# Kernel optimization log

Hardware: AMD Instinct MI355X
Metric: run time of the kernel (lower is better)

## Reference

```python
import jax, jax.numpy as jnp
import numpy as np

N = 100000
E = 1600000
B = 64
NUM_CLASSES = 10


def setup_inputs() -> dict:
    key = jax.random.key(0)
    ks = jax.random.split(key, 8)
    x = jax.random.normal(ks[0], (N, 5), dtype=jnp.float32)
    edge_index = jax.random.randint(ks[1], (2, E), 0, N, dtype=jnp.int64)
    batch = jnp.sort(jax.random.randint(ks[2], (N,), 0, B, dtype=jnp.int64))

    def glorot(k, fan_in, fan_out):
        s = jnp.sqrt(6.0 / (fan_in + fan_out)).astype(jnp.float32)
        return jax.random.uniform(k, (fan_in, fan_out), jnp.float32, -s, s)

    dims = [(5, 32), (32, 64), (64, 128), (128, 256)]
    Ws = [glorot(jax.random.fold_in(ks[3], i), a, b) for i, (a, b) in enumerate(dims)]
    bs = [jnp.zeros((b,), jnp.float32) for (_, b) in dims]
    fc1_w = glorot(ks[4], 256, 100)
    fc1_b = jnp.zeros((100,), jnp.float32)
    fc2_w = glorot(ks[5], 100, NUM_CLASSES)
    fc2_b = jnp.zeros((NUM_CLASSES,), jnp.float32)
    return {
        'x': x, 'edge_index': edge_index, 'batch': batch,
        'W1': Ws[0], 'b1': bs[0], 'W2': Ws[1], 'b2': bs[1],
        'W3': Ws[2], 'b3': bs[2], 'W4': Ws[3], 'b4': bs[3],
        'fc1_w': fc1_w, 'fc1_b': fc1_b, 'fc2_w': fc2_w, 'fc2_b': fc2_b,
    }


def _gcn_conv(x, W, b, src, dst, dinv):
    h = x @ W                                   # [N, out]
    norm = (dinv[src] * dinv[dst])[:, None]      # [E, 1]
    msg = h[src] * norm                          # gather + scale
    agg = jax.ops.segment_sum(msg, dst, num_segments=N)
    agg = agg + h * (dinv * dinv)[:, None]       # self-loop contribution
    return agg + b


def reference(x, edge_index, batch, W1, b1, W2, b2, W3, b3, W4, b4,
              fc1_w, fc1_b, fc2_w, fc2_b):
    src, dst = edge_index[0], edge_index[1]
    # degree including self-loop
    deg = jax.ops.segment_sum(jnp.ones((E,), jnp.float32), dst, num_segments=N) + 1.0
    dinv = jax.lax.rsqrt(deg)

    h = jax.nn.relu(_gcn_conv(x, W1, b1, src, dst, dinv))
    # mesh_unpool with pool target 0 -> identity
    h = jax.nn.relu(_gcn_conv(h, W2, b2, src, dst, dinv))
    h = jax.nn.relu(_gcn_conv(h, W3, b3, src, dst, dinv))
    h = jax.nn.relu(_gcn_conv(h, W4, b4, src, dst, dinv))

    # global mean pool over graphs
    sums = jax.ops.segment_sum(h, batch, num_segments=B)
    cnt = jax.ops.segment_sum(jnp.ones((N,), jnp.float32), batch, num_segments=B)
    pooled = sums / jnp.maximum(cnt, 1.0)[:, None]

    h = jax.nn.relu(pooled @ fc1_w + fc1_b)
    return jax.nn.log_softmax(h @ fc2_w + fc2_b, axis=-1)
```

## Files before the change

kernel.cpp:

```cpp
#include <hip/hip_runtime.h>
#include <hip/hip_bf16.h>
#include <cmath>

#define NN 100000
#define NE 1600000
#define NBATCH 64
#define NB 391
#define NBP 512
#define BCAP 6144
#define NPAD (NB * BCAP)

typedef __attribute__((ext_vector_type(8))) _Float16 f16x8;
typedef __attribute__((ext_vector_type(4))) float f32x4;
typedef __attribute__((ext_vector_type(2))) float f32x2;

__device__ __forceinline__ void atomAdd(float* p, float v) {
  unsafeAtomicAdd(p, v);
}

__device__ __forceinline__ unsigned char f2fp8(float f) {
  int pk = __builtin_amdgcn_cvt_pk_fp8_f32(f, f, 0, false);
  return (unsigned char)(pk & 0xff);
}

__device__ __forceinline__ void acc16(uint4 v, f32x2* acc) {
  acc[0] += __builtin_amdgcn_cvt_pk_f32_fp8(v.x, false);
  acc[1] += __builtin_amdgcn_cvt_pk_f32_fp8(v.x, true);
  acc[2] += __builtin_amdgcn_cvt_pk_f32_fp8(v.y, false);
  acc[3] += __builtin_amdgcn_cvt_pk_f32_fp8(v.y, true);
  acc[4] += __builtin_amdgcn_cvt_pk_f32_fp8(v.z, false);
  acc[5] += __builtin_amdgcn_cvt_pk_f32_fp8(v.z, true);
  acc[6] += __builtin_amdgcn_cvt_pk_f32_fp8(v.w, false);
  acc[7] += __builtin_amdgcn_cvt_pk_f32_fp8(v.w, true);
}

__global__ __launch_bounds__(256) void k_bin(const int* __restrict__ src,
    const int* __restrict__ dst, int* __restrict__ bucketCnt, unsigned* __restrict__ pairs,
    const float* __restrict__ W2, const float* __restrict__ W3, const float* __restrict__ W4,
    _Float16* __restrict__ Wt2, _Float16* __restrict__ Wt3, _Float16* __restrict__ Wt4) {
  __shared__ int hist[NBP];
  __shared__ int scn[NBP];
  __shared__ int ofs[NBP];
  __shared__ int gbase[NBP];
  __shared__ unsigned buf[4096];
  __shared__ unsigned short bufb[4096];
  const int base = blockIdx.x * 4096;
  const int n = (NE - base < 4096) ? NE - base : 4096;
  for (int i = threadIdx.x; i < NBP; i += 256) hist[i] = 0;
  __syncthreads();

  int myS[16], myD[16];
  int nloc = 0;
  for (int i = threadIdx.x, j = 0; i < n; i += 256, ++j) {
    myS[j] = src[base + i];
    myD[j] = dst[base + i];
    atomicAdd(&hist[myD[j] >> 8], 1);
    nloc = j + 1;
  }
  __syncthreads();

  scn[threadIdx.x] = hist[threadIdx.x];
  scn[threadIdx.x + 256] = hist[threadIdx.x + 256];
  __syncthreads();
  for (int off = 1; off < NBP; off <<= 1) {
    const int i0 = threadIdx.x, i1 = threadIdx.x + 256;
    int t0 = (i0 >= off) ? scn[i0 - off] : 0;
    int t1 = (i1 >= off) ? scn[i1 - off] : 0;
    __syncthreads();
    scn[i0] += t0;
    scn[i1] += t1;
    __syncthreads();
  }
  ofs[threadIdx.x] = scn[threadIdx.x] - hist[threadIdx.x];
  ofs[threadIdx.x + 256] = scn[threadIdx.x + 256] - hist[threadIdx.x + 256];
  for (int b = threadIdx.x; b < NB; b += 256) {
    int c = hist[b];
    if (c) gbase[b] = b * BCAP + atomicAdd(&bucketCnt[b], c);
  }
  __syncthreads();

  for (int j = 0; j < nloc; ++j) {
    int b = myD[j] >> 8;
    int slot = atomicAdd(&ofs[b], 1);
    buf[slot] = ((unsigned)myS[j] << 8) | ((unsigned)myD[j] & 255u);
    bufb[slot] = (unsigned short)b;
  }
  __syncthreads();

  for (int i = threadIdx.x; i < n; i += 256) {
    int b = (int)bufb[i];
    int ex = scn[b] - hist[b];
    pairs[gbase[b] + (i - ex)] = buf[i];
  }

  int idx = blockIdx.x * 256 + threadIdx.x;
  if (idx < 2048) {
    int k = idx / 64, m = idx - k * 64;
    Wt2[m * 32 + k] = (_Float16)W2[idx];
  } else if (idx < 10240) {
    int j = idx - 2048;
    int k = j / 128, m = j - k * 128;
    Wt3[m * 64 + k] = (_Float16)W3[j];
  } else if (idx < 43008) {
    int j = idx - 10240;
    int k = j / 256, m = j - k * 256;
    Wt4[m * 128 + k] = (_Float16)W4[j];
  }
}

__global__ __launch_bounds__(256) void k_cntfill(const unsigned* __restrict__ pairs,
    const int* __restrict__ bucketCnt, const int* __restrict__ batch,
    const float* __restrict__ x, int* __restrict__ rowbeg, int* __restrict__ rowend,
    float* __restrict__ dinv, int* __restrict__ csrc, float* __restrict__ pcnt,
    _Float16* __restrict__ xs8, unsigned char* __restrict__ F0,
    unsigned char* __restrict__ F1, unsigned char* __restrict__ F2) {
  __shared__ int c[256];
  __shared__ int scn[256];
  __shared__ int rowb[256];
  __shared__ int ofs[256];
  __shared__ int h[64];
  const int tid = threadIdx.x;
  c[tid] = 0; ofs[tid] = 0;
  if (tid < 64) h[tid] = 0;
  __syncthreads();
  const int b = blockIdx.x;
  const int s = b * BCAP;
  const int e = s + bucketCnt[b];
  for (int i = s + tid; i < e; i += 256) atomicAdd(&c[pairs[i] & 255u], 1);
  __syncthreads();
  const int v = c[tid];
  const int pv = (v + 3) & ~3;
  scn[tid] = pv;
  __syncthreads();
  for (int off = 1; off < 256; off <<= 1) {
    int t = (tid >= off) ? scn[tid - off] : 0;
    __syncthreads();
    scn[tid] += t;
    __syncthreads();
  }
  rowb[tid] = s + scn[tid] - pv;
  const int node = b * 256 + tid;
  rowbeg[node] = rowb[tid];
  rowend[node] = rowb[tid] + v;
  for (int p = v; p < pv; ++p) csrc[rowb[tid] + p] = NN;
  if (node < NN) {
    const float di = rsqrtf((float)v + 1.0f);
    dinv[node] = di;
    f16x8 o = {0, 0, 0, 0, 0, 0, 0, 0};
    o[0] = (_Float16)(x[(size_t)node * 5 + 0] * di);
    o[1] = (_Float16)(x[(size_t)node * 5 + 1] * di);
    o[2] = (_Float16)(x[(size_t)node * 5 + 2] * di);
    o[3] = (_Float16)(x[(size_t)node * 5 + 3] * di);
    o[4] = (_Float16)(x[(size_t)node * 5 + 4] * di);
    *(f16x8*)(xs8 + (size_t)node * 8) = o;
    atomicAdd(&h[batch[node]], 1);
  }
  if (b == 0 && tid < 15) {
    const uint4 z = make_uint4(0u, 0u, 0u, 0u);
    if (tid < 1)      ((uint4*)(xs8 + (size_t)NN * 8))[tid] = z;
    else if (tid < 3) ((uint4*)(F0 + (size_t)NN * 32))[tid - 1] = z;
    else if (tid < 7) ((uint4*)(F1 + (size_t)NN * 64))[tid - 3] = z;
    else              ((uint4*)(F2 + (size_t)NN * 128))[tid - 7] = z;
  }
  __syncthreads();
  for (int i = s + tid; i < e; i += 256) {
    unsigned p = pairs[i];
    int t = (int)(p & 255u);
    int pos = rowb[t] + atomicAdd(&ofs[t], 1);
    csrc[pos] = (int)(p >> 8);
  }
  if (tid < 64 && h[tid]) atomAdd(&pcnt[tid], (float)h[tid]);
}

struct MegaArgs {
  const _Float16* xs8;
  const int* rowbeg; const int* rowend; const int* csrc;
  const float* dinv;
  const float* W1; const float* b1;
  unsigned char* F0;
  const _Float16* Wt2; const float* b2;
  unsigned char* F1;
  const _Float16* Wt3; const float* b3;
  unsigned char* F2;
  const _Float16* Wt4; const float* b4;
  const int* batch; float* pooled; const float* pcnt;
  const float* fc1w; const float* fc1b; const float* fc2w; const float* fc2b;
  float* out;
};

__global__ __launch_bounds__(256) void kw_l1(MegaArgs a) {
  __shared__ float w_s[160];
  __shared__ float b_s[32];
  const int tid = threadIdx.x;
  if (tid < 160) w_s[tid] = a.W1[tid];
  if (tid < 32) b_s[tid] = a.b1[tid];
  __syncthreads();
  const int r = blockIdx.x * 256 + tid;
  if (r >= NN) return;
  const float di = a.dinv[r];
  const _Float16* xs = a.xs8;
  f16x8 av = *(const f16x8*)(xs + (size_t)r * 8);
  f16x8 a0 = {0,0,0,0,0,0,0,0}, a1 = {0,0,0,0,0,0,0,0};
  f16x8 a2 = {0,0,0,0,0,0,0,0}, a3 = {0,0,0,0,0,0,0,0};
  const int eb = a.rowbeg[r];
  const int nIt = (a.rowend[r] - eb + 3) >> 2;
  const uint4* cp = (const uint4*)(a.csrc + eb);
  uint4 i0 = cp[0], i1 = cp[1];
  int it = 0;
  for (; it + 2 <= nIt; it += 2) {
    const f16x8 f0 = *(const f16x8*)(xs + (size_t)i0.x * 8);
    const f16x8 f1 = *(const f16x8*)(xs + (size_t)i0.y * 8);
    const f16x8 f2 = *(const f16x8*)(xs + (size_t)i0.z * 8);
    const f16x8 f3 = *(const f16x8*)(xs + (size_t)i0.w * 8);
    const f16x8 f4 = *(const f16x8*)(xs + (size_t)i1.x * 8);
    const f16x8 f5 = *(const f16x8*)(xs + (size_t)i1.y * 8);
    const f16x8 f6 = *(const f16x8*)(xs + (size_t)i1.z * 8);
    const f16x8 f7 = *(const f16x8*)(xs + (size_t)i1.w * 8);
    const uint4 n0 = cp[it + 2], n1 = cp[it + 3];
    a0 += f0; a1 += f1; a2 += f2; a3 += f3;
    a0 += f4; a1 += f5; a2 += f6; a3 += f7;
    i0 = n0; i1 = n1;
  }
  if (it < nIt) {
    const f16x8 f0 = *(const f16x8*)(xs + (size_t)i0.x * 8);
    const f16x8 f1 = *(const f16x8*)(xs + (size_t)i0.y * 8);
    const f16x8 f2 = *(const f16x8*)(xs + (size_t)i0.z * 8);
    const f16x8 f3 = *(const f16x8*)(xs + (size_t)i0.w * 8);
    a0 += f0; a1 += f1; a2 += f2; a3 += f3;
  }
  a0 += a1; a2 += a3; a0 += a2; av += a0;
  const float f0 = (float)av[0] * di, f1 = (float)av[1] * di, f2 = (float)av[2] * di,
              f3 = (float)av[3] * di, f4 = (float)av[4] * di;
  float v[32];
#pragma unroll
  for (int j = 0; j < 32; ++j) {
    float s = b_s[j] + f0 * w_s[j] + f1 * w_s[32 + j] + f2 * w_s[64 + j]
                     + f3 * w_s[96 + j] + f4 * w_s[128 + j];
    v[j] = fmaxf(s, 0.f) * di;
  }
  unsigned u[8];
#pragma unroll
  for (int g2 = 0; g2 < 8; ++g2) {
    int uu = 0;
    uu = __builtin_amdgcn_cvt_pk_fp8_f32(v[4 * g2],     v[4 * g2 + 1], uu, false);
    uu = __builtin_amdgcn_cvt_pk_fp8_f32(v[4 * g2 + 2], v[4 * g2 + 3], uu, true);
    u[g2] = (unsigned)uu;
  }
  uint4* op = (uint4*)(a.F0 + (size_t)r * 32);
  op[0] = make_uint4(u[0], u[1], u[2], u[3]);
  op[1] = make_uint4(u[4], u[5], u[6], u[7]);
}

template<int K, int M, int MODE, int THREADS>
__global__ __launch_bounds__(THREADS) void kw_fgemm(MegaArgs a,
    const unsigned char* __restrict__ in,
    const _Float16* __restrict__ Wt, const float* __restrict__ bias,
    unsigned char* __restrict__ outp) {
  constexpr int KC = 32;
  constexpr int KP = K + 8;
  constexpr int NW = THREADS / 64;
  constexpr int MW = M / NW;
  constexpr int CTW = MW / 16;
  constexpr int TPR = K / 16;
  constexpr int RPP = THREADS / TPR;
  constexpr int NPASS = 64 / RPP;
  __shared__ _Float16 a_s[64 * KP];
  const int tid = threadIdx.x;
  const int wave = tid >> 6, lane = tid & 63;
  const int m16 = lane & 15, q = lane >> 4;
  const int r0 = blockIdx.x * 64;

  {
    const int rowg = tid / TPR;
    const int c = (tid % TPR) * 16;
    const unsigned char* bp = in + c;
#pragma unroll
    for (int pass = 0; pass < NPASS; ++pass) {
      const int row = pass * RPP + rowg;
      const int r = r0 + row;
      f32x2 acc8[8];
#pragma unroll
      for (int i = 0; i < 8; ++i) acc8[i] = (f32x2){0.f, 0.f};
      float di = 0.f;
      if (r < NN) {
        di = a.dinv[r];
        const int eb = a.rowbeg[r];
        const int nIt = (a.rowend[r] - eb + 3) >> 2;
        const uint4* cp = (const uint4*)(a.csrc + eb);
        uint4 i0 = cp[0], i1 = cp[1];
        acc16(*(const uint4*)(bp + (size_t)r * K), acc8);
        int it = 0;
        for (; it + 2 <= nIt; it += 2) {
          const uint4 f0 = *(const uint4*)(bp + (size_t)i0.x * K);
          const uint4 f1 = *(const uint4*)(bp + (size_t)i0.y * K);
          const uint4 f2 = *(const uint4*)(bp + (size_t)i0.z * K);
          const uint4 f3 = *(const uint4*)(bp + (size_t)i0.w * K);
          const uint4 f4 = *(const uint4*)(bp + (size_t)i1.x * K);
          const uint4 f5 = *(const uint4*)(bp + (size_t)i1.y * K);
          const uint4 f6 = *(const uint4*)(bp + (size_t)i1.z * K);
          const uint4 f7 = *(const uint4*)(bp + (size_t)i1.w * K);
          const uint4 n0 = cp[it + 2], n1 = cp[it + 3];
          acc16(f0, acc8); acc16(f1, acc8); acc16(f2, acc8); acc16(f3, acc8);
          acc16(f4, acc8); acc16(f5, acc8); acc16(f6, acc8); acc16(f7, acc8);
          i0 = n0; i1 = n1;
        }
        if (it < nIt) {
          const uint4 f0 = *(const uint4*)(bp + (size_t)i0.x * K);
          const uint4 f1 = *(const uint4*)(bp + (size_t)i0.y * K);
          const uint4 f2 = *(const uint4*)(bp + (size_t)i0.z * K);
          const uint4 f3 = *(const uint4*)(bp + (size_t)i0.w * K);
          acc16(f0, acc8); acc16(f1, acc8); acc16(f2, acc8); acc16(f3, acc8);
        }
      }
      _Float16 h[16];
#pragma unroll
      for (int i = 0; i < 8; ++i) {
        h[2 * i]     = (_Float16)(acc8[i].x * di);
        h[2 * i + 1] = (_Float16)(acc8[i].y * di);
      }
      *(uint4*)&a_s[row * KP + c]     = *(uint4*)&h[0];
      *(uint4*)&a_s[row * KP + c + 8] = *(uint4*)&h[8];
    }
  }
  __syncthreads();

  f32x4 acc[4][CTW];
#pragma unroll
  for (int rt = 0; rt < 4; ++rt)
#pragma unroll
    for (int ct = 0; ct < CTW; ++ct) acc[rt][ct] = (f32x4){0.f, 0.f, 0.f, 0.f};

  const _Float16* wp = Wt + (size_t)(wave * MW) * K + q * 8;
#pragma unroll
  for (int kc = 0; kc < K; kc += KC) {
    f16x8 bfr[CTW];
#pragma unroll
    for (int ct = 0; ct < CTW; ++ct)
      bfr[ct] = *(const f16x8*)(wp + (size_t)(ct * 16 + m16) * K + kc);
#pragma unroll
    for (int rt = 0; rt < 4; ++rt) {
      f16x8 afr = *(const f16x8*)&a_s[(rt * 16 + m16) * KP + kc + q * 8];
#pragma unroll
      for (int ct = 0; ct < CTW; ++ct)
        acc[rt][ct] = __builtin_amdgcn_mfma_f32_16x16x32_f16(afr, bfr[ct], acc[rt][ct], 0, 0, 0);
    }
  }

  if constexpr (MODE == 1) {
    const int rlast = (r0 + 63 < NN) ? r0 + 63 : NN - 1;
    const int bmin = a.batch[r0];
    const int bmax = a.batch[rlast];
    int rowb[4][4];
#pragma unroll
    for (int rt = 0; rt < 4; ++rt)
#pragma unroll
      for (int reg = 0; reg < 4; ++reg) {
        const int row = r0 + rt * 16 + q * 4 + reg;
        rowb[rt][reg] = (row < NN) ? a.batch[row] : -1;
      }
#pragma unroll
    for (int ct = 0; ct < CTW; ++ct) {
      const int col = wave * MW + ct * 16 + m16;
      const float bv = bias[col];
      for (int b = bmin; b <= bmax; ++b) {
        float s = 0.f;
#pragma unroll
        for (int rt = 0; rt < 4; ++rt)
#pragma unroll
          for (int reg = 0; reg < 4; ++reg)
            if (rowb[rt][reg] == b) s += fmaxf(acc[rt][ct][reg] + bv, 0.f);
        s += __shfl_xor(s, 16);
        s += __shfl_xor(s, 32);
        if (q == 0) atomAdd(&a.pooled[b * M + col], s);
      }
    }
  } else {
    float dsc[4][4];
#pragma unroll
    for (int rt = 0; rt < 4; ++rt)
#pragma unroll
      for (int reg = 0; reg < 4; ++reg) {
        const int row = r0 + rt * 16 + q * 4 + reg;
        dsc[rt][reg] = (row < NN) ? a.dinv[row] : 0.f;
      }
#pragma unroll
    for (int rt = 0; rt < 4; ++rt) {
#pragma unroll
      for (int ct = 0; ct < CTW; ++ct) {
        const int col = wave * MW + ct * 16 + m16;
        const float bv = bias[col];
#pragma unroll
        for (int reg = 0; reg < 4; ++reg) {
          const int row = r0 + rt * 16 + q * 4 + reg;
          if (row < NN) {
            float vv = fmaxf(acc[rt][ct][reg] + bv, 0.f) * dsc[rt][reg];
            outp[(size_t)row * M + col] = f2fp8(vv);
          }
        }
      }
    }
  }
}

__global__ __launch_bounds__(256) void kw_mlp(MegaArgs a) {
  __shared__ float p[256];
  __shared__ float h1[100];
  __shared__ float lo[10];
  const int tid = threadIdx.x;
  const int b = blockIdx.x;
  const float inv = 1.0f / fmaxf(a.pcnt[b], 1.0f);
  p[tid] = a.pooled[b * 256 + tid] * inv;
  __syncthreads();
  for (int j = tid; j < 100; j += 256) {
    float s = a.fc1b[j];
    for (int k = 0; k < 256; ++k) s += p[k] * a.fc1w[k * 100 + j];
    h1[j] = fmaxf(s, 0.f);
  }
  __syncthreads();
  if (tid < 10) {
    float s = a.fc2b[tid];
    for (int k = 0; k < 100; ++k) s += h1[k] * a.fc2w[k * 10 + tid];
    lo[tid] = s;
  }
  __syncthreads();
  if (tid == 0) {
    float m = lo[0];
    for (int j = 1; j < 10; ++j) m = fmaxf(m, lo[j]);
    float ssum = 0.f;
    for (int j = 0; j < 10; ++j) ssum += expf(lo[j] - m);
    float lse = m + logf(ssum);
    for (int j = 0; j < 10; ++j) a.out[b * 10 + j] = lo[j] - lse;
  }
}

extern "C" void kernel_launch(void* const* d_in, const int* in_sizes, int n_in,
                              void* d_out, int out_size, void* d_ws, size_t ws_size,
                              hipStream_t stream) {
  const float* x     = (const float*)d_in[0];
  const int*   ei    = (const int*)d_in[1];
  const int*   batch = (const int*)d_in[2];
  const float* W1 = (const float*)d_in[3];  const float* b1 = (const float*)d_in[4];
  const float* W2 = (const float*)d_in[5];  const float* b2 = (const float*)d_in[6];
  const float* W3 = (const float*)d_in[7];  const float* b3 = (const float*)d_in[8];
  const float* W4 = (const float*)d_in[9];  const float* b4 = (const float*)d_in[10];
  const float* fc1w = (const float*)d_in[11]; const float* fc1b = (const float*)d_in[12];
  const float* fc2w = (const float*)d_in[13]; const float* fc2b = (const float*)d_in[14];
  float* out = (float*)d_out;

  const int* src = ei;
  const int* dst = ei + NE;

  float* ws = (float*)d_ws;
  float* pooled = ws;
  float* pcnt   = pooled + 16384;
  int*   bucketCnt = (int*)(pcnt + 64);
  float* dinv   = (float*)(bucketCnt + 512);
  int*   rowbeg = (int*)(dinv + 100352);
  int*   rowend = rowbeg + 100352;
  int*   csrc   = rowend + 100352;
  unsigned* pairs = (unsigned*)(csrc + NPAD);
  _Float16* xs8 = (_Float16*)(pairs + NPAD);
  unsigned char* F0 = (unsigned char*)(xs8 + 800768);
  unsigned char* F1 = F0 + 3200128;
  unsigned char* F2 = F1 + 6400128;
  _Float16* Wt2 = (_Float16*)(F2 + 12800128);
  _Float16* Wt3 = Wt2 + 32 * 64;
  _Float16* Wt4 = Wt3 + 64 * 128;

  (void)hipMemsetAsync(pooled, 0, (16384 + 64 + 512) * sizeof(float), stream);
  k_bin<<<(NE + 4095) / 4096, 256, 0, stream>>>(src, dst, bucketCnt, pairs,
                                                W2, W3, W4, Wt2, Wt3, Wt4);
  k_cntfill<<<NB, 256, 0, stream>>>(pairs, bucketCnt, batch, x,
                                    rowbeg, rowend, dinv, csrc, pcnt, xs8,
                                    F0, F1, F2);

  MegaArgs m;
  m.xs8 = xs8; m.rowbeg = rowbeg; m.rowend = rowend; m.csrc = csrc;
  m.dinv = dinv;
  m.W1 = W1; m.b1 = b1; m.F0 = F0;
  m.Wt2 = Wt2; m.b2 = b2; m.F1 = F1;
  m.Wt3 = Wt3; m.b3 = b3; m.F2 = F2;
  m.Wt4 = Wt4; m.b4 = b4;
  m.batch = batch; m.pooled = pooled; m.pcnt = pcnt;
  m.fc1w = fc1w; m.fc1b = fc1b; m.fc2w = fc2w; m.fc2b = fc2b;
  m.out = out;

  const int gtile = (NN + 63) / 64;
  kw_l1<<<(NN + 255) / 256, 256, 0, stream>>>(m);
  kw_fgemm<32, 64, 0, 128><<<gtile, 128, 0, stream>>>(m, F0, Wt2, b2, F1);
  kw_fgemm<64, 128, 0, 256><<<gtile, 256, 0, stream>>>(m, F1, Wt3, b3, F2);
  kw_fgemm<128, 256, 1, 256><<<gtile, 256, 0, stream>>>(m, F2, Wt4, b4, nullptr);
  kw_mlp<<<NBATCH, 256, 0, stream>>>(m);
}
```

Measured before the change: 277.5 us.

## Split layers 3-4 into column-sliced gather kernel plus separate MFMA GEMM kernel

For the two widest GCN layers, the fused gather+GEMM kernel is replaced by two kernels. A column-sliced gather kernel aggregates neighbour fp8 features in 32-column slices per block and writes the normalized aggregate to a new fp8 buffer. A plain GEMM kernel then reloads that buffer into shared memory as fp16 and runs the MFMA plus epilogue. The aim is more parallelism and better cache locality in the gather, since each block now touches only a narrow column slice. The cost is an extra round trip of the aggregate through global memory, an added fp8 rounding, and reading the CSR index list once per slice instead of once. Index loads also switch to nontemporal loads throughout.

```diff
diff --git a/kernel.cpp b/kernel.cpp
--- a/kernel.cpp
+++ b/kernel.cpp
@@ -9,10 +9,12 @@
 #define NBP 512
 #define BCAP 6144
 #define NPAD (NB * BCAP)
+#define RT128 782
 
 typedef __attribute__((ext_vector_type(8))) _Float16 f16x8;
 typedef __attribute__((ext_vector_type(4))) float f32x4;
 typedef __attribute__((ext_vector_type(2))) float f32x2;
+typedef __attribute__((ext_vector_type(4))) unsigned int u32x4;
 
 __device__ __forceinline__ void atomAdd(float* p, float v) {
   unsafeAtomicAdd(p, v);
@@ -21,6 +23,15 @@
 __device__ __forceinline__ unsigned char f2fp8(float f) {
   int pk = __builtin_amdgcn_cvt_pk_fp8_f32(f, f, 0, false);
   return (unsigned char)(pk & 0xff);
+}
+
+__device__ __forceinline__ u32x4 ldnt(const u32x4* p) {
+  return __builtin_nontemporal_load(p);
+}
+
+__device__ __forceinline__ void stnt(unsigned char* p, uint4 v) {
+  u32x4 t = {v.x, v.y, v.z, v.w};
+  __builtin_nontemporal_store(t, (u32x4*)p);
 }
 
 __device__ __forceinline__ void acc16(uint4 v, f32x2* acc) {
@@ -32,6 +43,18 @@
   acc[5] += __builtin_amdgcn_cvt_pk_f32_fp8(v.z, true);
   acc[6] += __builtin_amdgcn_cvt_pk_f32_fp8(v.w, false);
   acc[7] += __builtin_amdgcn_cvt_pk_f32_fp8(v.w, true);
+}
+
+__device__ __forceinline__ void fp8x16_to_f16(uint4 v, _Float16* h) {
+  f32x2 t;
+  t = __builtin_amdgcn_cvt_pk_f32_fp8(v.x, false); h[0] = (_Float16)t.x;  h[1] = (_Float16)t.y;
+  t = __builtin_amdgcn_cvt_pk_f32_fp8(v.x, true);  h[2] = (_Float16)t.x;  h[3] = (_Float16)t.y;
+  t = __builtin_amdgcn_cvt_pk_f32_fp8(v.y, false); h[4] = (_Float16)t.x;  h[5] = (_Float16)t.y;
+  t = __builtin_amdgcn_cvt_pk_f32_fp8(v.y, true);  h[6] = (_Float16)t.x;  h[7] = (_Float16)t.y;
+  t = __builtin_amdgcn_cvt_pk_f32_fp8(v.z, false); h[8] = (_Float16)t.x;  h[9] = (_Float16)t.y;
+  t = __builtin_amdgcn_cvt_pk_f32_fp8(v.z, true);  h[10] = (_Float16)t.x; h[11] = (_Float16)t.y;
+  t = __builtin_amdgcn_cvt_pk_f32_fp8(v.w, false); h[12] = (_Float16)t.x; h[13] = (_Float16)t.y;
+  t = __builtin_amdgcn_cvt_pk_f32_fp8(v.w, true);  h[14] = (_Float16)t.x; h[15] = (_Float16)t.y;
 }
 
 __global__ __launch_bounds__(256) void k_bin(const int* __restrict__ src,
@@ -183,6 +206,7 @@
   const _Float16* Wt3; const float* b3;
   unsigned char* F2;
   const _Float16* Wt4; const float* b4;
+  unsigned char* AG8;
   const int* batch; float* pooled; const float* pcnt;
   const float* fc1w; const float* fc1b; const float* fc2w; const float* fc2b;
   float* out;
@@ -204,8 +228,8 @@
   f16x8 a2 = {0,0,0,0,0,0,0,0}, a3 = {0,0,0,0,0,0,0,0};
   const int eb = a.rowbeg[r];
   const int nIt = (a.rowend[r] - eb + 3) >> 2;
-  const uint4* cp = (const uint4*)(a.csrc + eb);
-  uint4 i0 = cp[0], i1 = cp[1];
+  const u32x4* cp = (const u32x4*)(a.csrc + eb);
+  u32x4 i0 = ldnt(cp), i1 = ldnt(cp + 1);
   int it = 0;
   for (; it + 2 <= nIt; it += 2) {
     const f16x8 f0 = *(const f16x8*)(xs + (size_t)i0.x * 8);
@@ -216,7 +240,7 @@
     const f16x8 f5 = *(const f16x8*)(xs + (size_t)i1.y * 8);
     const f16x8 f6 = *(const f16x8*)(xs + (size_t)i1.z * 8);
     const f16x8 f7 = *(const f16x8*)(xs + (size_t)i1.w * 8);
-    const uint4 n0 = cp[it + 2], n1 = cp[it + 3];
+    const u32x4 n0 = ldnt(cp + it + 2), n1 = ldnt(cp + it + 3);
     a0 += f0; a1 += f1; a2 += f2; a3 += f3;
     a0 += f4; a1 += f5; a2 += f6; a3 += f7;
     i0 = n0; i1 = n1;
@@ -286,8 +310,8 @@
         di = a.dinv[r];
         const int eb = a.rowbeg[r];
         const int nIt = (a.rowend[r] - eb + 3) >> 2;
-        const uint4* cp = (const uint4*)(a.csrc + eb);
-        uint4 i0 = cp[0], i1 = cp[1];
+        const u32x4* cp = (const u32x4*)(a.csrc + eb);
+        u32x4 i0 = ldnt(cp), i1 = ldnt(cp + 1);
         acc16(*(const uint4*)(bp + (size_t)r * K), acc8);
         int it = 0;
         for (; it + 2 <= nIt; it += 2) {
@@ -299,7 +323,7 @@
           const uint4 f5 = *(const uint4*)(bp + (size_t)i1.y * K);
           const uint4 f6 = *(const uint4*)(bp + (size_t)i1.z * K);
           const uint4 f7 = *(const uint4*)(bp + (size_t)i1.w * K);
-          const uint4 n0 = cp[it + 2], n1 = cp[it + 3];
+          const u32x4 n0 = ldnt(cp + it + 2), n1 = ldnt(cp + it + 3);
           acc16(f0, acc8); acc16(f1, acc8); acc16(f2, acc8); acc16(f3, acc8);
           acc16(f4, acc8); acc16(f5, acc8); acc16(f6, acc8); acc16(f7, acc8);
           i0 = n0; i1 = n1;
@@ -321,6 +345,164 @@
       *(uint4*)&a_s[row * KP + c]     = *(uint4*)&h[0];
       *(uint4*)&a_s[row * KP + c + 8] = *(uint4*)&h[8];
     }
+  }
+  __syncthreads();
+
+  f32x4 acc[4][CTW];
+#pragma unroll
+  for (int rt = 0; rt < 4; ++rt)
+#pragma unroll
+    for (int ct = 0; ct < CTW; ++ct) acc[rt][ct] = (f32x4){0.f, 0.f, 0.f, 0.f};
+
+  const _Float16* wp = Wt + (size_t)(wave * MW) * K + q * 8;
+#pragma unroll
+  for (int kc = 0; kc < K; kc += KC) {
+    f16x8 bfr[CTW];
+#pragma unroll
+    for (int ct = 0; ct < CTW; ++ct)
+      bfr[ct] = *(const f16x8*)(wp + (size_t)(ct * 16 + m16) * K + kc);
+#pragma unroll
+    for (int rt = 0; rt < 4; ++rt) {
+      f16x8 afr = *(const f16x8*)&a_s[(rt * 16 + m16) * KP + kc + q * 8];
+#pragma unroll
+      for (int ct = 0; ct < CTW; ++ct)
+        acc[rt][ct] = __builtin_amdgcn_mfma_f32_16x16x32_f16(afr, bfr[ct], acc[rt][ct], 0, 0, 0);
+    }
+  }
+
+  if constexpr (MODE == 1) {
+    const int rlast = (r0 + 63 < NN) ? r0 + 63 : NN - 1;
+    const int bmin = a.batch[r0];
+    const int bmax = a.batch[rlast];
+    int rowb[4][4];
+#pragma unroll
+    for (int rt = 0; rt < 4; ++rt)
+#pragma unroll
+      for (int reg = 0; reg < 4; ++reg) {
+        const int row = r0 + rt * 16 + q * 4 + reg;
+        rowb[rt][reg] = (row < NN) ? a.batch[row] : -1;
+      }
+#pragma unroll
+    for (int ct = 0; ct < CTW; ++ct) {
+      const int col = wave * MW + ct * 16 + m16;
+      const float bv = bias[col];
+      for (int b = bmin; b <= bmax; ++b) {
+        float s = 0.f;
+#pragma unroll
+        for (int rt = 0; rt < 4; ++rt)
+#pragma unroll
+          for (int reg = 0; reg < 4; ++reg)
+            if (rowb[rt][reg] == b) s += fmaxf(acc[rt][ct][reg] + bv, 0.f);
+        s += __shfl_xor(s, 16);
+        s += __shfl_xor(s, 32);
+        if (q == 0) atomAdd(&a.pooled[b * M + col], s);
+      }
+    }
+  } else {
+    float dsc[4][4];
+#pragma unroll
+    for (int rt = 0; rt < 4; ++rt)
+#pragma unroll
+      for (int reg = 0; reg < 4; ++reg) {
+        const int row = r0 + rt * 16 + q * 4 + reg;
+        dsc[rt][reg] = (row < NN) ? a.dinv[row] : 0.f;
+      }
+#pragma unroll
+    for (int rt = 0; rt < 4; ++rt) {
+#pragma unroll
+      for (int ct = 0; ct < CTW; ++ct) {
+        const int col = wave * MW + ct * 16 + m16;
+        const float bv = bias[col];
+#pragma unroll
+        for (int reg = 0; reg < 4; ++reg) {
+          const int row = r0 + rt * 16 + q * 4 + reg;
+          if (row < NN) {
+            float vv = fmaxf(acc[rt][ct][reg] + bv, 0.f) * dsc[rt][reg];
+            outp[(size_t)row * M + col] = f2fp8(vv);
+          }
+        }
+      }
+    }
+  }
+}
+
+template<int K>
+__global__ __launch_bounds__(256) void kq_gather(MegaArgs a,
+    const unsigned char* __restrict__ in, unsigned char* __restrict__ outp) {
+  const int bid = blockIdx.x;
+  const int qq = bid / RT128;
+  const int tile = bid - qq * RT128;
+  const int r = tile * 128 + (threadIdx.x >> 1);
+  if (r >= NN) return;
+  const int c = qq * 32 + (threadIdx.x & 1) * 16;
+  const unsigned char* bp = in + c;
+  f32x2 acc8[8];
+#pragma unroll
+  for (int i = 0; i < 8; ++i) acc8[i] = (f32x2){0.f, 0.f};
+  const float di = a.dinv[r];
+  const int eb = a.rowbeg[r];
+  const int nIt = (a.rowend[r] - eb + 3) >> 2;
+  const u32x4* cp = (const u32x4*)(a.csrc + eb);
+  u32x4 i0 = ldnt(cp), i1 = ldnt(cp + 1);
+  acc16(*(const uint4*)(bp + (size_t)r * K), acc8);
+  int it = 0;
+  for (; it + 2 <= nIt; it += 2) {
+    const uint4 f0 = *(const uint4*)(bp + (size_t)i0.x * K);
+    const uint4 f1 = *(const uint4*)(bp + (size_t)i0.y * K);
+    const uint4 f2 = *(const uint4*)(bp + (size_t)i0.z * K);
+    const uint4 f3 = *(const uint4*)(bp + (size_t)i0.w * K);
+    const uint4 f4 = *(const uint4*)(bp + (size_t)i1.x * K);
+    const uint4 f5 = *(const uint4*)(bp + (size_t)i1.y * K);
+    const uint4 f6 = *(const uint4*)(bp + (size_t)i1.z * K);
+    const uint4 f7 = *(const uint4*)(bp + (size_t)i1.w * K);
+    const u32x4 n0 = ldnt(cp + it + 2), n1 = ldnt(cp + it + 3);
+    acc16(f0, acc8); acc16(f1, acc8); acc16(f2, acc8); acc16(f3, acc8);
+    acc16(f4, acc8); acc16(f5, acc8); acc16(f6, acc8); acc16(f7, acc8);
+    i0 = n0; i1 = n1;
+  }
+  if (it < nIt) {
+    const uint4 f0 = *(const uint4*)(bp + (size_t)i0.x * K);
+    const uint4 f1 = *(const uint4*)(bp + (size_t)i0.y * K);
+    const uint4 f2 = *(const uint4*)(bp + (size_t)i0.z * K);
+    const uint4 f3 = *(const uint4*)(bp + (size_t)i0.w * K);
+    acc16(f0, acc8); acc16(f1, acc8); acc16(f2, acc8); acc16(f3, acc8);
+  }
+  int w0 = __builtin_amdgcn_cvt_pk_fp8_f32(acc8[0].x * di, acc8[0].y * di, 0, false);
+  w0     = __builtin_amdgcn_cvt_pk_fp8_f32(acc8[1].x * di, acc8[1].y * di, w0, true);
+  int w1 = __builtin_amdgcn_cvt_pk_fp8_f32(acc8[2].x * di, acc8[2].y * di, 0, false);
+  w1     = __builtin_amdgcn_cvt_pk_fp8_f32(acc8[3].x * di, acc8[3].y * di, w1, true);
+  int w2 = __builtin_amdgcn_cvt_pk_fp8_f32(acc8[4].x * di, acc8[4].y * di, 0, false);
+  w2     = __builtin_amdgcn_cvt_pk_fp8_f32(acc8[5].x * di, acc8[5].y * di, w2, true);
+  int w3 = __builtin_amdgcn_cvt_pk_fp8_f32(acc8[6].x * di, acc8[6].y * di, 0, false);
+  w3     = __builtin_amdgcn_cvt_pk_fp8_f32(acc8[7].x * di, acc8[7].y * di, w3, true);
+  stnt(outp + (size_t)r * K + c, make_uint4((unsigned)w0, (unsigned)w1,
+                                            (unsigned)w2, (unsigned)w3));
+}
+
+template<int K, int M, int MODE>
+__global__ __launch_bounds__(256) void kg_gemm(MegaArgs a,
+    const unsigned char* __restrict__ in,
+    const _Float16* __restrict__ Wt, const float* __restrict__ bias,
+    unsigned char* __restrict__ outp) {
+  constexpr int KC = 32;
+  constexpr int KP = K + 8;
+  constexpr int MW = M / 4;
+  constexpr int CTW = MW / 16;
+  constexpr int C16 = K / 16;
+  __shared__ _Float16 a_s[64 * KP];
+  const int tid = threadIdx.x;
+  const int wave = tid >> 6, lane = tid & 63;
+  const int m16 = lane & 15, q = lane >> 4;
+  const int r0 = blockIdx.x * 64;
+
+  for (int idx = tid; idx < 64 * C16; idx += 256) {
+    int row = idx / C16, cc = (idx % C16) * 16;
+    uint4 v = {0u, 0u, 0u, 0u};
+    if (r0 + row < NN) v = *(const uint4*)(in + (size_t)(r0 + row) * K + cc);
+    _Float16 h[16];
+    fp8x16_to_f16(v, h);
+    *(uint4*)&a_s[row * KP + cc]     = *(uint4*)&h[0];
+    *(uint4*)&a_s[row * KP + cc + 8] = *(uint4*)&h[8];
   }
   __syncthreads();
 
@@ -463,7 +645,8 @@
   unsigned char* F0 = (unsigned char*)(xs8 + 800768);
   unsigned char* F1 = F0 + 3200128;
   unsigned char* F2 = F1 + 6400128;
-  _Float16* Wt2 = (_Float16*)(F2 + 12800128);
+  unsigned char* AG8 = F2 + 12800128;
+  _Float16* Wt2 = (_Float16*)(AG8 + 12800128);
   _Float16* Wt3 = Wt2 + 32 * 64;
   _Float16* Wt4 = Wt3 + 64 * 128;
 
@@ -480,7 +663,7 @@
   m.W1 = W1; m.b1 = b1; m.F0 = F0;
   m.Wt2 = Wt2; m.b2 = b2; m.F1 = F1;
   m.Wt3 = Wt3; m.b3 = b3; m.F2 = F2;
-  m.Wt4 = Wt4; m.b4 = b4;
+  m.Wt4 = Wt4; m.b4 = b4; m.AG8 = AG8;
   m.batch = batch; m.pooled = pooled; m.pcnt = pcnt;
   m.fc1w = fc1w; m.fc1b = fc1b; m.fc2w = fc2w; m.fc2b = fc2b;
   m.out = out;
@@ -488,7 +671,9 @@
   const int gtile = (NN + 63) / 64;
   kw_l1<<<(NN + 255) / 256, 256, 0, stream>>>(m);
   kw_fgemm<32, 64, 0, 128><<<gtile, 128, 0, stream>>>(m, F0, Wt2, b2, F1);
-  kw_fgemm<64, 128, 0, 256><<<gtile, 256, 0, stream>>>(m, F1, Wt3, b3, F2);
-  kw_fgemm<128, 256, 1, 256><<<gtile, 256, 0, stream>>>(m, F2, Wt4, b4, nullptr);
+  kq_gather<64><<<RT128 * 2, 256, 0, stream>>>(m, F1, AG8);
+  kg_gemm<64, 128, 0><<<gtile, 256, 0, stream>>>(m, AG8, Wt3, b3, F2);
+  kq_gather<128><<<RT128 * 4, 256, 0, stream>>>(m, F2, AG8);
+  kg_gemm<128, 256, 1><<<gtile, 256, 0, stream>>>(m, AG8, Wt4, b4, nullptr);
   kw_mlp<<<NBATCH, 256, 0, stream>>>(m);
 }
```

Result: slower. 364.0 us (+31.1%).
